# Optimization experiments

Hardware: AMD Instinct MI355X
Metric: run time of the kernel (lower is better)

## Reference

```python
import jax, jax.numpy as jnp
import numpy as np

MARGIN = 0.3
NORM_EPS = 1e-12  # torch F.normalize default eps


def setup_inputs() -> dict:
    key = jax.random.key(0)
    k1, k2 = jax.random.split(key)
    embeddings = jax.random.normal(k1, (8192, 128), dtype=jnp.float32)
    labels = jax.random.randint(k2, (8192,), 0, 128, dtype=jnp.int64)
    return {"embeddings": embeddings, "labels": labels}


def _triplet_loss(embeddings, labels):
    # L2-normalize rows (torch F.normalize: x / max(||x||, eps))
    norm = jnp.linalg.norm(embeddings, axis=1, keepdims=True)
    e = embeddings / jnp.maximum(norm, NORM_EPS)

    # pairwise squared Euclidean via gram matrix
    dot = e @ e.T                     # [B, B]
    sq = jnp.diagonal(dot)            # [B]
    d2 = jnp.clip(sq[None, :] - 2.0 * dot + sq[:, None], 0.0)
    zmask = (d2 == 0.0).astype(d2.dtype)
    dist = jnp.sqrt(d2 + zmask * 1e-16) * (1.0 - zmask)  # [B, B]

    # hard mining, fully vectorized over rows
    same = labels[:, None] == labels[None, :]
    eye = jnp.eye(labels.shape[0], dtype=bool)
    pos_mask = same & ~eye
    neg_mask = ~same

    dist_ap = jnp.max(jnp.where(pos_mask, dist, -jnp.inf), axis=1)  # hardest positive
    dist_an = jnp.min(jnp.where(neg_mask, dist, jnp.inf), axis=1)   # hardest negative

    valid = pos_mask.any(axis=1) & neg_mask.any(axis=1)
    # MarginRankingLoss(margin)(dist_an, dist_ap, y=1) = mean relu(dist_ap - dist_an + margin)
    per_row = jnp.maximum(dist_ap - dist_an + MARGIN, 0.0)
    n_valid = jnp.maximum(jnp.sum(valid), 1).astype(dist.dtype)
    loss = jnp.sum(jnp.where(valid, per_row, 0.0)) / n_valid
    return jnp.where(valid.any(), loss, jnp.zeros((), dist.dtype))


def reference(embeddings, labels):
    return _triplet_loss(embeddings, labels)
```

## Files before the change

kernel.cpp:

```cpp
#include <hip/hip_runtime.h>
#include <cmath>

#define BN 8192
#define DIM 128
#define MARGIN_F 0.3f
#define NSPLIT 8
#define CPS 1024
#define NT 8
#define IMAX 0x7FFFFFFF
#define IMIN 0x80000000

typedef __attribute__((ext_vector_type(4))) int i32x4;

__device__ __forceinline__ int imin3(int a, int b, int c) { return min(a, min(b, c)); }
__device__ __forceinline__ int imax3(int a, int b, int c) { return max(a, max(b, c)); }

__global__ __launch_bounds__(256) void norm_cvt_k(
    const float* __restrict__ emb, float* __restrict__ sqv, unsigned short* __restrict__ EnQ16,
    int* __restrict__ ap_f, int* __restrict__ an_f)
{
  int gt = blockIdx.x * blockDim.x + threadIdx.x;
  if (gt < BN) { ap_f[gt] = IMAX; an_f[gt] = IMIN; }

  int w = gt >> 6;
  int lane = threadIdx.x & 63;
  if (w >= BN) return;
  float2 v = *reinterpret_cast<const float2*>(&emb[w * DIM + lane * 2]);
  float s = v.x * v.x + v.y * v.y;
  #pragma unroll
  for (int off = 32; off > 0; off >>= 1) s += __shfl_xor(s, off);
  float iv = 1.0f / fmaxf(sqrtf(s), 1e-12f);
  if (lane == 0) sqv[w] = s * iv * iv;
  int q0 = (int)rintf(127.0f * v.x * iv);
  int q1 = (int)rintf(127.0f * v.y * iv);
  unsigned short us = (unsigned short)((q0 & 255) | ((q1 & 255) << 8));
  int g = lane >> 3;
  EnQ16[(g * BN + w) * 8 + (lane & 7)] = us;
}

__global__ __launch_bounds__(256, 2) void gram_mine_mfma_k(
    const char* __restrict__ EnQ, const int* __restrict__ lab,
    int* __restrict__ ap_f, int* __restrict__ an_f)
{
  __shared__ __align__(16) char Bs[2][16384];

  const int tid = threadIdx.x;
  const int w = tid >> 6, l = tid & 63;
  const int wr = w >> 1, wc = w & 1;
  const int lrow = l & 15, lkg = l >> 4;

  const int rowBase = blockIdx.x * 128 + wr * 64;
  const int panel   = blockIdx.y * CPS;

  i32x4 a[4][2];
  #pragma unroll
  for (int mi = 0; mi < 4; ++mi)
    #pragma unroll
    for (int kk = 0; kk < 2; ++kk)
      a[mi][kk] = *reinterpret_cast<const i32x4*>(
          EnQ + (((size_t)((kk << 2) + lkg) * BN + rowBase + mi * 16 + lrow) << 4));

  unsigned rlbp[4];
  #pragma unroll
  for (int mi = 0; mi < 4; ++mi) {
    int rb = rowBase + mi * 16 + lkg * 4;
    rlbp[mi] = (unsigned)(lab[rb] & 255) | ((unsigned)(lab[rb + 1] & 255) << 8) |
               ((unsigned)(lab[rb + 2] & 255) << 16) | ((unsigned)(lab[rb + 3] & 255) << 24);
  }

  int ap[4][4], an[4][4];
  #pragma unroll
  for (int mi = 0; mi < 4; ++mi)
    #pragma unroll
    for (int r = 0; r < 4; ++r) { ap[mi][r] = IMAX; an[mi][r] = IMIN; }

  const i32x4 zf = {0, 0, 0, 0};

  auto stage = [&](int buf, int colTile) {
    #pragma unroll
    for (int i = 0; i < 4; ++i) {
      int s0 = (w << 8) + (i << 6);
      int s  = s0 + l;
      const char* gp = EnQ + (((size_t)(s >> 7) * BN + colTile + (s & 127)) << 4);
      __builtin_amdgcn_global_load_lds(
          (const __attribute__((address_space(1))) void*)gp,
          (__attribute__((address_space(3))) void*)(&Bs[buf][s0 * 16]),
          16, 0, 0);
    }
  };

  stage(0, panel);
  __syncthreads();

  int cur = 0;
  #pragma unroll 1
  for (int ct = 0; ct < NT; ++ct) {
    const int colTile = panel + ct * 128;
    const int colBase = colTile + wc * 64;

    if (ct + 1 < NT) stage(cur ^ 1, colTile + 128);

    int clb[4];
    #pragma unroll
    for (int ni = 0; ni < 4; ++ni) clb[ni] = lab[colBase + ni * 16 + lrow];

    const bool diag = (rowBase == colBase);

    #pragma unroll
    for (int half = 0; half < 2; ++half) {
      const int n0 = half * 2, n1 = half * 2 + 1;

      i32x4 acc[4][2];
      {
        i32x4 b[2];
        #pragma unroll
        for (int n = 0; n < 2; ++n)
          b[n] = *reinterpret_cast<const i32x4*>(
              &Bs[cur][((0 + lkg) * 128 + wc * 64 + (n0 + n) * 16 + lrow) * 16]);
        #pragma unroll
        for (int mi = 0; mi < 4; ++mi)
          #pragma unroll
          for (int n = 0; n < 2; ++n)
            acc[mi][n] = __builtin_amdgcn_mfma_i32_16x16x64_i8(
                a[mi][0], b[n], zf, 0, 0, 0);
      }
      {
        i32x4 b[2];
        #pragma unroll
        for (int n = 0; n < 2; ++n)
          b[n] = *reinterpret_cast<const i32x4*>(
              &Bs[cur][((4 + lkg) * 128 + wc * 64 + (n0 + n) * 16 + lrow) * 16]);
        #pragma unroll
        for (int mi = 0; mi < 4; ++mi)
          #pragma unroll
          for (int n = 0; n < 2; ++n)
            acc[mi][n] = __builtin_amdgcn_mfma_i32_16x16x64_i8(
                a[mi][1], b[n], acc[mi][n], 0, 0, 0);
      }

      if (diag) {
        #pragma unroll
        for (int mi = 0; mi < 4; ++mi)
          #pragma unroll
          for (int r = 0; r < 4; ++r) {
            int rl = (int)((rlbp[mi] >> (r * 8)) & 255u);
            int rloc = mi * 16 + lkg * 4 + r;
            int d0 = acc[mi][0][r], d1 = acc[mi][1][r];
            bool s0 = (rl == clb[n0]), s1 = (rl == clb[n1]);
            bool e0 = (rloc == n0 * 16 + lrow), e1 = (rloc == n1 * 16 + lrow);
            int p0 = (s0 && !e0) ? d0 : IMAX;
            int p1 = (s1 && !e1) ? d1 : IMAX;
            int q0 = s0 ? IMIN : d0;
            int q1 = s1 ? IMIN : d1;
            ap[mi][r] = imin3(ap[mi][r], p0, p1);
            an[mi][r] = imax3(an[mi][r], q0, q1);
          }
      } else {
        #pragma unroll
        for (int mi = 0; mi < 4; ++mi)
          #pragma unroll
          for (int r = 0; r < 4; ++r) {
            int rl = (int)((rlbp[mi] >> (r * 8)) & 255u);
            int d0 = acc[mi][0][r], d1 = acc[mi][1][r];
            bool s0 = (rl == clb[n0]), s1 = (rl == clb[n1]);
            int p0 = s0 ? d0 : IMAX;
            int p1 = s1 ? d1 : IMAX;
            int q0 = s0 ? IMIN : d0;
            int q1 = s1 ? IMIN : d1;
            ap[mi][r] = imin3(ap[mi][r], p0, p1);
            an[mi][r] = imax3(an[mi][r], q0, q1);
          }
      }
    }

    __syncthreads();
    cur ^= 1;
  }

  #pragma unroll
  for (int mi = 0; mi < 4; ++mi)
    #pragma unroll
    for (int r = 0; r < 4; ++r) {
      int p = ap[mi][r], n = an[mi][r];
      #pragma unroll
      for (int off = 1; off < 16; off <<= 1) {
        p = min(p, __shfl_xor(p, off));
        n = max(n, __shfl_xor(n, off));
      }
      if (lrow == 0) {
        int rg = rowBase + mi * 16 + lkg * 4 + r;
        atomicMin(&ap_f[rg], p);
        atomicMax(&an_f[rg], n);
      }
    }
}

__global__ __launch_bounds__(1024) void finalize_k(
    const int* __restrict__ ap_f, const int* __restrict__ an_f,
    const float* __restrict__ sqv, float* __restrict__ out)
{
  int t = threadIdx.x;
  float sum = 0.f, cnt = 0.f;
  #pragma unroll
  for (int i = 0; i < BN / 1024; ++i) {
    int r = i * 1024 + t;
    int apt = ap_f[r], ant = an_f[r];
    if (apt != IMAX && ant != IMIN) {
      const float sc = 2.0f / (127.0f * 127.0f);
      float rs1 = sqv[r] + 1.0f;
      float dap = sqrtf(fmaxf(fmaf(-sc, (float)apt, rs1), 0.f));
      float dan = sqrtf(fmaxf(fmaf(-sc, (float)ant, rs1), 0.f));
      sum += fmaxf(dap - dan + MARGIN_F, 0.f);
      cnt += 1.f;
    }
  }
  #pragma unroll
  for (int off = 32; off > 0; off >>= 1) {
    sum += __shfl_xor(sum, off);
    cnt += __shfl_xor(cnt, off);
  }
  __shared__ float ssum[16], scnt[16];
  int wv = t >> 6;
  if ((t & 63) == 0) { ssum[wv] = sum; scnt[wv] = cnt; }
  __syncthreads();
  if (t == 0) {
    float s = 0.f, c = 0.f;
    #pragma unroll
    for (int i = 0; i < 16; ++i) { s += ssum[i]; c += scnt[i]; }
    out[0] = (c > 0.f) ? (s / c) : 0.f;
  }
}

extern "C" void kernel_launch(void* const* d_in, const int* in_sizes, int n_in,
                              void* d_out, int out_size, void* d_ws, size_t ws_size,
                              hipStream_t stream)
{
  const float* emb = (const float*)d_in[0];
  const int*   lab = (const int*)d_in[1];
  float* out = (float*)d_out;
  float* ws  = (float*)d_ws;

  float* sqv  = ws;
  int*   ap_f = (int*)(sqv + BN);
  int*   an_f = ap_f + BN;
  char*  EnQ  = (char*)(an_f + BN);

  norm_cvt_k<<<dim3(BN / 4), 256, 0, stream>>>(emb, sqv, (unsigned short*)EnQ, ap_f, an_f);
  gram_mine_mfma_k<<<dim3(BN / 128, NSPLIT), 256, 0, stream>>>(EnQ, lab, ap_f, an_f);
  finalize_k<<<dim3(1), 1024, 0, stream>>>(ap_f, an_f, sqv, out);
}
```

Before: 35.82 us.

## Counting-sort rows by label so tiles without shared labels skip positive mining

Adds a histogram kernel and scatters normalized, quantized rows into label-sorted order. In the gram kernel, each 64x64 wave tile compares its row and column label ranges, and tiles with no overlap update only the hardest-negative max, skipping label loads and comparisons. This is meant to cut the per-element mining ALU work that follows the MFMAs. In exchange it adds a serial single-block prefix kernel, atomics in the normalize kernel, and nondeterministic row order within each bin; the final mean does not depend on row order.

New measurement: 53.16 us. +48.4%, slower.

```diff
diff --git a/kernel.cpp b/kernel.cpp
--- a/kernel.cpp
+++ b/kernel.cpp
@@ -7,6 +7,7 @@
 #define NSPLIT 8
 #define CPS 1024
 #define NT 8
+#define NLAB 128
 #define IMAX 0x7FFFFFFF
 #define IMIN 0x80000000
 
@@ -15,8 +16,35 @@
 __device__ __forceinline__ int imin3(int a, int b, int c) { return min(a, min(b, c)); }
 __device__ __forceinline__ int imax3(int a, int b, int c) { return max(a, max(b, c)); }
 
+__global__ __launch_bounds__(1024) void sort_prep_k(
+    const int* __restrict__ lab, int* __restrict__ binStart, int* __restrict__ binCur)
+{
+  __shared__ int h[16][NLAB];
+  int t = threadIdx.x, wv = t >> 6;
+  for (int i = t; i < 16 * NLAB; i += 1024) (&h[0][0])[i] = 0;
+  __syncthreads();
+  for (int i = t; i < BN; i += 1024) atomicAdd(&h[wv][lab[i] & (NLAB - 1)], 1);
+  __syncthreads();
+  if (t < NLAB) {
+    int s = 0;
+    #pragma unroll
+    for (int w2 = 0; w2 < 16; ++w2) s += h[w2][t];
+    h[0][t] = s;
+  }
+  __syncthreads();
+  if (t == 0) {
+    int acc = 0;
+    for (int b = 0; b < NLAB; ++b) {
+      int c = h[0][b];
+      binStart[b] = acc; binCur[b] = acc; acc += c;
+    }
+  }
+}
+
 __global__ __launch_bounds__(256) void norm_cvt_k(
-    const float* __restrict__ emb, float* __restrict__ sqv, unsigned short* __restrict__ EnQ16,
+    const float* __restrict__ emb, const int* __restrict__ lab,
+    float* __restrict__ sqvS, unsigned short* __restrict__ EnQ16,
+    int* __restrict__ labS, int* __restrict__ binCur,
     int* __restrict__ ap_f, int* __restrict__ an_f)
 {
   int gt = blockIdx.x * blockDim.x + threadIdx.x;
@@ -25,21 +53,27 @@
   int w = gt >> 6;
   int lane = threadIdx.x & 63;
   if (w >= BN) return;
+
+  int lb = 0, dst = 0;
+  if (lane == 0) { lb = lab[w]; dst = atomicAdd(&binCur[lb], 1); }
+  dst = __shfl(dst, 0);
+  lb  = __shfl(lb, 0);
+
   float2 v = *reinterpret_cast<const float2*>(&emb[w * DIM + lane * 2]);
   float s = v.x * v.x + v.y * v.y;
   #pragma unroll
   for (int off = 32; off > 0; off >>= 1) s += __shfl_xor(s, off);
   float iv = 1.0f / fmaxf(sqrtf(s), 1e-12f);
-  if (lane == 0) sqv[w] = s * iv * iv;
+  if (lane == 0) { sqvS[dst] = s * iv * iv; labS[dst] = lb; }
   int q0 = (int)rintf(127.0f * v.x * iv);
   int q1 = (int)rintf(127.0f * v.y * iv);
   unsigned short us = (unsigned short)((q0 & 255) | ((q1 & 255) << 8));
   int g = lane >> 3;
-  EnQ16[(g * BN + w) * 8 + (lane & 7)] = us;
+  EnQ16[(g * BN + dst) * 8 + (lane & 7)] = us;
 }
 
 __global__ __launch_bounds__(256, 2) void gram_mine_mfma_k(
-    const char* __restrict__ EnQ, const int* __restrict__ lab,
+    const char* __restrict__ EnQ, const int* __restrict__ labS,
     int* __restrict__ ap_f, int* __restrict__ an_f)
 {
   __shared__ __align__(16) char Bs[2][16384];
@@ -52,6 +86,8 @@
   const int rowBase = blockIdx.x * 128 + wr * 64;
   const int panel   = blockIdx.y * CPS;
 
+  const int rLo = labS[rowBase], rHi = labS[rowBase + 63];
+
   i32x4 a[4][2];
   #pragma unroll
   for (int mi = 0; mi < 4; ++mi)
@@ -64,8 +100,8 @@
   #pragma unroll
   for (int mi = 0; mi < 4; ++mi) {
     int rb = rowBase + mi * 16 + lkg * 4;
-    rlbp[mi] = (unsigned)(lab[rb] & 255) | ((unsigned)(lab[rb + 1] & 255) << 8) |
-               ((unsigned)(lab[rb + 2] & 255) << 16) | ((unsigned)(lab[rb + 3] & 255) << 24);
+    rlbp[mi] = (unsigned)(labS[rb] & 255) | ((unsigned)(labS[rb + 1] & 255) << 8) |
+               ((unsigned)(labS[rb + 2] & 255) << 16) | ((unsigned)(labS[rb + 3] & 255) << 24);
   }
 
   int ap[4][4], an[4][4];
@@ -100,11 +136,15 @@
 
     if (ct + 1 < NT) stage(cur ^ 1, colTile + 128);
 
+    const int cLo = labS[colBase], cHi = labS[colBase + 63];
+    const bool mixed = (cHi >= rLo) && (cLo <= rHi);
+    const bool diag  = (rowBase == colBase);
+
     int clb[4];
-    #pragma unroll
-    for (int ni = 0; ni < 4; ++ni) clb[ni] = lab[colBase + ni * 16 + lrow];
-
-    const bool diag = (rowBase == colBase);
+    if (mixed) {
+      #pragma unroll
+      for (int ni = 0; ni < 4; ++ni) clb[ni] = labS[colBase + ni * 16 + lrow];
+    }
 
     #pragma unroll
     for (int half = 0; half < 2; ++half) {
@@ -138,7 +178,13 @@
                 a[mi][1], b[n], acc[mi][n], 0, 0, 0);
       }
 
-      if (diag) {
+      if (!mixed) {
+        #pragma unroll
+        for (int mi = 0; mi < 4; ++mi)
+          #pragma unroll
+          for (int r = 0; r < 4; ++r)
+            an[mi][r] = imax3(an[mi][r], acc[mi][0][r], acc[mi][1][r]);
+      } else if (diag) {
         #pragma unroll
         for (int mi = 0; mi < 4; ++mi)
           #pragma unroll
@@ -197,7 +243,7 @@
 
 __global__ __launch_bounds__(1024) void finalize_k(
     const int* __restrict__ ap_f, const int* __restrict__ an_f,
-    const float* __restrict__ sqv, float* __restrict__ out)
+    const float* __restrict__ sqvS, float* __restrict__ out)
 {
   int t = threadIdx.x;
   float sum = 0.f, cnt = 0.f;
@@ -207,7 +253,7 @@
     int apt = ap_f[r], ant = an_f[r];
     if (apt != IMAX && ant != IMIN) {
       const float sc = 2.0f / (127.0f * 127.0f);
-      float rs1 = sqv[r] + 1.0f;
+      float rs1 = sqvS[r] + 1.0f;
       float dap = sqrtf(fmaxf(fmaf(-sc, (float)apt, rs1), 0.f));
       float dan = sqrtf(fmaxf(fmaf(-sc, (float)ant, rs1), 0.f));
       sum += fmaxf(dap - dan + MARGIN_F, 0.f);
@@ -240,12 +286,17 @@
   float* out = (float*)d_out;
   float* ws  = (float*)d_ws;
 
-  float* sqv  = ws;
-  int*   ap_f = (int*)(sqv + BN);
-  int*   an_f = ap_f + BN;
-  char*  EnQ  = (char*)(an_f + BN);
-
-  norm_cvt_k<<<dim3(BN / 4), 256, 0, stream>>>(emb, sqv, (unsigned short*)EnQ, ap_f, an_f);
-  gram_mine_mfma_k<<<dim3(BN / 128, NSPLIT), 256, 0, stream>>>(EnQ, lab, ap_f, an_f);
-  finalize_k<<<dim3(1), 1024, 0, stream>>>(ap_f, an_f, sqv, out);
-}
+  float* sqvS     = ws;
+  int*   ap_f     = (int*)(sqvS + BN);
+  int*   an_f     = ap_f + BN;
+  int*   labS     = an_f + BN;
+  int*   binStart = labS + BN;
+  int*   binCur   = binStart + NLAB;
+  char*  EnQ      = (char*)(binCur + NLAB + 16);
+
+  sort_prep_k<<<dim3(1), 1024, 0, stream>>>(lab, binStart, binCur);
+  norm_cvt_k<<<dim3(BN / 4), 256, 0, stream>>>(emb, lab, sqvS, (unsigned short*)EnQ,
+                                               labS, binCur, ap_f, an_f);
+  gram_mine_mfma_k<<<dim3(BN / 128, NSPLIT), 256, 0, stream>>>(EnQ, labS, ap_f, an_f);
+  finalize_k<<<dim3(1), 1024, 0, stream>>>(ap_f, an_f, sqvS, out);
+}
```

## Exploit Gram symmetry with upper-triangular tiles and column-side mining

Applied to the files above, without the earlier changes.

Replaces the row-block by column-panel grid with one block per upper-triangular 128x128 tile pair, using the symmetry of the Gram matrix to mine both rows and columns from each tile. This roughly halves the MFMA and mining work, and each block now loads its B operand straight from global memory instead of double-buffering it through LDS. Column labels are prepacked in the normalize kernel, and atomics for empty positive sets are skipped. The cost is many more small blocks with no intra-block loop, plus extra column reductions and atomics per off-diagonal tile.

Result: slower. 56.80 us (+58.6%).

```diff
diff --git a/kernel.cpp b/kernel.cpp
--- a/kernel.cpp
+++ b/kernel.cpp
@@ -4,9 +4,8 @@
 #define BN 8192
 #define DIM 128
 #define MARGIN_F 0.3f
-#define NSPLIT 8
-#define CPS 1024
-#define NT 8
+#define NRB 64
+#define NTILE (NRB * (NRB + 1) / 2)
 #define IMAX 0x7FFFFFFF
 #define IMIN 0x80000000
 
@@ -16,11 +15,17 @@
 __device__ __forceinline__ int imax3(int a, int b, int c) { return max(a, max(b, c)); }
 
 __global__ __launch_bounds__(256) void norm_cvt_k(
-    const float* __restrict__ emb, float* __restrict__ sqv, unsigned short* __restrict__ EnQ16,
-    int* __restrict__ ap_f, int* __restrict__ an_f)
+    const float* __restrict__ emb, const int* __restrict__ lab,
+    float* __restrict__ sqv, unsigned short* __restrict__ EnQ16,
+    unsigned* __restrict__ LP, int* __restrict__ ap_f, int* __restrict__ an_f)
 {
   int gt = blockIdx.x * blockDim.x + threadIdx.x;
   if (gt < BN) { ap_f[gt] = IMAX; an_f[gt] = IMIN; }
+  if (gt < 2048) {
+    int base = (gt >> 4) * 64 + (gt & 15);
+    LP[gt] = (unsigned)(lab[base] & 255) | ((unsigned)(lab[base + 16] & 255) << 8) |
+             ((unsigned)(lab[base + 32] & 255) << 16) | ((unsigned)(lab[base + 48] & 255) << 24);
+  }
 
   int w = gt >> 6;
   int lane = threadIdx.x & 63;
@@ -38,19 +43,26 @@
   EnQ16[(g * BN + w) * 8 + (lane & 7)] = us;
 }
 
-__global__ __launch_bounds__(256, 2) void gram_mine_mfma_k(
+__global__ __launch_bounds__(256, 2) void tri_gram_mine_k(
     const char* __restrict__ EnQ, const int* __restrict__ lab,
+    const unsigned* __restrict__ LP,
     int* __restrict__ ap_f, int* __restrict__ an_f)
 {
-  __shared__ __align__(16) char Bs[2][16384];
-
   const int tid = threadIdx.x;
   const int w = tid >> 6, l = tid & 63;
   const int wr = w >> 1, wc = w & 1;
   const int lrow = l & 15, lkg = l >> 4;
 
-  const int rowBase = blockIdx.x * 128 + wr * 64;
-  const int panel   = blockIdx.y * CPS;
+  const int idx = blockIdx.x;
+  int R = (int)((129.0f - sqrtf(16641.0f - 8.0f * (float)idx)) * 0.5f);
+  while (((R + 1) * (129 - (R + 1))) / 2 <= idx) ++R;
+  while ((R * (129 - R)) / 2 > idx) --R;
+  const int C = R + (idx - (R * (129 - R)) / 2);
+
+  const int rowBase = R * 128 + wr * 64;
+  const int colBase = C * 128 + wc * 64;
+  const bool diagW  = (rowBase == colBase);
+  const bool doCol  = (R != C);
 
   i32x4 a[4][2];
   #pragma unroll
@@ -60,121 +72,117 @@
       a[mi][kk] = *reinterpret_cast<const i32x4*>(
           EnQ + (((size_t)((kk << 2) + lkg) * BN + rowBase + mi * 16 + lrow) << 4));
 
-  unsigned rlbp[4];
+  int rlv[4][4];
   #pragma unroll
   for (int mi = 0; mi < 4; ++mi) {
     int rb = rowBase + mi * 16 + lkg * 4;
-    rlbp[mi] = (unsigned)(lab[rb] & 255) | ((unsigned)(lab[rb + 1] & 255) << 8) |
-               ((unsigned)(lab[rb + 2] & 255) << 16) | ((unsigned)(lab[rb + 3] & 255) << 24);
-  }
+    #pragma unroll
+    for (int r = 0; r < 4; ++r) rlv[mi][r] = lab[rb + r] & 255;
+  }
+
+  const unsigned LPv = LP[(colBase >> 6) * 16 + lrow];
+  const int l0 = (int)(LPv & 255u),         l1 = (int)((LPv >> 8) & 255u);
+  const int l2 = (int)((LPv >> 16) & 255u), l3 = (int)(LPv >> 24);
 
   int ap[4][4], an[4][4];
   #pragma unroll
   for (int mi = 0; mi < 4; ++mi)
     #pragma unroll
     for (int r = 0; r < 4; ++r) { ap[mi][r] = IMAX; an[mi][r] = IMIN; }
+  int cmin[4], cmax[4];
+  #pragma unroll
+  for (int n = 0; n < 4; ++n) { cmin[n] = IMAX; cmax[n] = IMIN; }
 
   const i32x4 zf = {0, 0, 0, 0};
 
-  auto stage = [&](int buf, int colTile) {
-    #pragma unroll
-    for (int i = 0; i < 4; ++i) {
-      int s0 = (w << 8) + (i << 6);
-      int s  = s0 + l;
-      const char* gp = EnQ + (((size_t)(s >> 7) * BN + colTile + (s & 127)) << 4);
-      __builtin_amdgcn_global_load_lds(
-          (const __attribute__((address_space(1))) void*)gp,
-          (__attribute__((address_space(3))) void*)(&Bs[buf][s0 * 16]),
-          16, 0, 0);
-    }
+  const char* bp0 = EnQ + (((size_t)lkg * BN + colBase + lrow) << 4);
+  const char* bp1 = bp0 + ((size_t)BN << 6);
+
+  i32x4 b0[2][2], b1[2][2];
+  #pragma unroll
+  for (int n = 0; n < 2; ++n) {
+    b0[0][n] = *reinterpret_cast<const i32x4*>(bp0 + n * 256);
+    b0[1][n] = *reinterpret_cast<const i32x4*>(bp1 + n * 256);
+    b1[0][n] = *reinterpret_cast<const i32x4*>(bp0 + (2 + n) * 256);
+    b1[1][n] = *reinterpret_cast<const i32x4*>(bp1 + (2 + n) * 256);
+  }
+
+  i32x4 accA[4][2], accB[4][2];
+  #pragma unroll
+  for (int mi = 0; mi < 4; ++mi)
+    #pragma unroll
+    for (int n = 0; n < 2; ++n)
+      accA[mi][n] = __builtin_amdgcn_mfma_i32_16x16x64_i8(a[mi][0], b0[0][n], zf, 0, 0, 0);
+  #pragma unroll
+  for (int mi = 0; mi < 4; ++mi)
+    #pragma unroll
+    for (int n = 0; n < 2; ++n)
+      accA[mi][n] = __builtin_amdgcn_mfma_i32_16x16x64_i8(a[mi][1], b0[1][n], accA[mi][n], 0, 0, 0);
+  #pragma unroll
+  for (int mi = 0; mi < 4; ++mi)
+    #pragma unroll
+    for (int n = 0; n < 2; ++n)
+      accB[mi][n] = __builtin_amdgcn_mfma_i32_16x16x64_i8(a[mi][0], b1[0][n], zf, 0, 0, 0);
+  #pragma unroll
+  for (int mi = 0; mi < 4; ++mi)
+    #pragma unroll
+    for (int n = 0; n < 2; ++n)
+      accB[mi][n] = __builtin_amdgcn_mfma_i32_16x16x64_i8(a[mi][1], b1[1][n], accB[mi][n], 0, 0, 0);
+
+  auto mineRow = [&](const i32x4 (&A)[4][2], int la, int lb) {
+    #pragma unroll
+    for (int mi = 0; mi < 4; ++mi)
+      #pragma unroll
+      for (int r = 0; r < 4; ++r) {
+        int d0 = A[mi][0][r], d1 = A[mi][1][r];
+        bool s0 = (rlv[mi][r] == la), s1 = (rlv[mi][r] == lb);
+        int p0 = s0 ? d0 : IMAX, p1 = s1 ? d1 : IMAX;
+        int q0 = s0 ? IMIN : d0, q1 = s1 ? IMIN : d1;
+        ap[mi][r] = imin3(ap[mi][r], p0, p1);
+        an[mi][r] = imax3(an[mi][r], q0, q1);
+      }
   };
-
-  stage(0, panel);
-  __syncthreads();
-
-  int cur = 0;
-  #pragma unroll 1
-  for (int ct = 0; ct < NT; ++ct) {
-    const int colTile = panel + ct * 128;
-    const int colBase = colTile + wc * 64;
-
-    if (ct + 1 < NT) stage(cur ^ 1, colTile + 128);
-
-    int clb[4];
-    #pragma unroll
-    for (int ni = 0; ni < 4; ++ni) clb[ni] = lab[colBase + ni * 16 + lrow];
-
-    const bool diag = (rowBase == colBase);
-
-    #pragma unroll
-    for (int half = 0; half < 2; ++half) {
-      const int n0 = half * 2, n1 = half * 2 + 1;
-
-      i32x4 acc[4][2];
-      {
-        i32x4 b[2];
-        #pragma unroll
-        for (int n = 0; n < 2; ++n)
-          b[n] = *reinterpret_cast<const i32x4*>(
-              &Bs[cur][((0 + lkg) * 128 + wc * 64 + (n0 + n) * 16 + lrow) * 16]);
-        #pragma unroll
-        for (int mi = 0; mi < 4; ++mi)
-          #pragma unroll
-          for (int n = 0; n < 2; ++n)
-            acc[mi][n] = __builtin_amdgcn_mfma_i32_16x16x64_i8(
-                a[mi][0], b[n], zf, 0, 0, 0);
-      }
-      {
-        i32x4 b[2];
-        #pragma unroll
-        for (int n = 0; n < 2; ++n)
-          b[n] = *reinterpret_cast<const i32x4*>(
-              &Bs[cur][((4 + lkg) * 128 + wc * 64 + (n0 + n) * 16 + lrow) * 16]);
-        #pragma unroll
-        for (int mi = 0; mi < 4; ++mi)
-          #pragma unroll
-          for (int n = 0; n < 2; ++n)
-            acc[mi][n] = __builtin_amdgcn_mfma_i32_16x16x64_i8(
-                a[mi][1], b[n], acc[mi][n], 0, 0, 0);
-      }
-
-      if (diag) {
-        #pragma unroll
-        for (int mi = 0; mi < 4; ++mi)
-          #pragma unroll
-          for (int r = 0; r < 4; ++r) {
-            int rl = (int)((rlbp[mi] >> (r * 8)) & 255u);
-            int rloc = mi * 16 + lkg * 4 + r;
-            int d0 = acc[mi][0][r], d1 = acc[mi][1][r];
-            bool s0 = (rl == clb[n0]), s1 = (rl == clb[n1]);
-            bool e0 = (rloc == n0 * 16 + lrow), e1 = (rloc == n1 * 16 + lrow);
-            int p0 = (s0 && !e0) ? d0 : IMAX;
-            int p1 = (s1 && !e1) ? d1 : IMAX;
-            int q0 = s0 ? IMIN : d0;
-            int q1 = s1 ? IMIN : d1;
-            ap[mi][r] = imin3(ap[mi][r], p0, p1);
-            an[mi][r] = imax3(an[mi][r], q0, q1);
-          }
-      } else {
-        #pragma unroll
-        for (int mi = 0; mi < 4; ++mi)
-          #pragma unroll
-          for (int r = 0; r < 4; ++r) {
-            int rl = (int)((rlbp[mi] >> (r * 8)) & 255u);
-            int d0 = acc[mi][0][r], d1 = acc[mi][1][r];
-            bool s0 = (rl == clb[n0]), s1 = (rl == clb[n1]);
-            int p0 = s0 ? d0 : IMAX;
-            int p1 = s1 ? d1 : IMAX;
-            int q0 = s0 ? IMIN : d0;
-            int q1 = s1 ? IMIN : d1;
-            ap[mi][r] = imin3(ap[mi][r], p0, p1);
-            an[mi][r] = imax3(an[mi][r], q0, q1);
-          }
-      }
-    }
-
-    __syncthreads();
-    cur ^= 1;
+  auto mineRowCol = [&](const i32x4 (&A)[4][2], int la, int lb,
+                        int& cmA, int& cxA, int& cmB, int& cxB) {
+    #pragma unroll
+    for (int mi = 0; mi < 4; ++mi)
+      #pragma unroll
+      for (int r = 0; r < 4; ++r) {
+        int d0 = A[mi][0][r], d1 = A[mi][1][r];
+        bool s0 = (rlv[mi][r] == la), s1 = (rlv[mi][r] == lb);
+        int p0 = s0 ? d0 : IMAX, p1 = s1 ? d1 : IMAX;
+        int q0 = s0 ? IMIN : d0, q1 = s1 ? IMIN : d1;
+        ap[mi][r] = imin3(ap[mi][r], p0, p1);
+        an[mi][r] = imax3(an[mi][r], q0, q1);
+        cmA = min(cmA, p0); cxA = max(cxA, q0);
+        cmB = min(cmB, p1); cxB = max(cxB, q1);
+      }
+  };
+  auto mineDiag = [&](const i32x4 (&A)[4][2], int la, int lb, int c0, int c1) {
+    #pragma unroll
+    for (int mi = 0; mi < 4; ++mi)
+      #pragma unroll
+      for (int r = 0; r < 4; ++r) {
+        int rloc = mi * 16 + lkg * 4 + r;
+        int d0 = A[mi][0][r], d1 = A[mi][1][r];
+        bool s0 = (rlv[mi][r] == la), s1 = (rlv[mi][r] == lb);
+        bool e0 = (rloc == c0), e1 = (rloc == c1);
+        int p0 = (s0 && !e0) ? d0 : IMAX, p1 = (s1 && !e1) ? d1 : IMAX;
+        int q0 = s0 ? IMIN : d0, q1 = s1 ? IMIN : d1;
+        ap[mi][r] = imin3(ap[mi][r], p0, p1);
+        an[mi][r] = imax3(an[mi][r], q0, q1);
+      }
+  };
+
+  if (diagW) {
+    mineDiag(accA, l0, l1, lrow, 16 + lrow);
+    mineDiag(accB, l2, l3, 32 + lrow, 48 + lrow);
+  } else if (doCol) {
+    mineRowCol(accA, l0, l1, cmin[0], cmax[0], cmin[1], cmax[1]);
+    mineRowCol(accB, l2, l3, cmin[2], cmax[2], cmin[3], cmax[3]);
+  } else {
+    mineRow(accA, l0, l1);
+    mineRow(accB, l2, l3);
   }
 
   #pragma unroll
@@ -189,10 +197,24 @@
       }
       if (lrow == 0) {
         int rg = rowBase + mi * 16 + lkg * 4 + r;
-        atomicMin(&ap_f[rg], p);
+        if (p != IMAX) atomicMin(&ap_f[rg], p);
         atomicMax(&an_f[rg], n);
       }
     }
+
+  if (doCol) {
+    #pragma unroll
+    for (int n = 0; n < 4; ++n) {
+      int cm = cmin[n], cx = cmax[n];
+      cm = min(cm, __shfl_xor(cm, 16)); cm = min(cm, __shfl_xor(cm, 32));
+      cx = max(cx, __shfl_xor(cx, 16)); cx = max(cx, __shfl_xor(cx, 32));
+      if (lkg == 0) {
+        int cg = colBase + n * 16 + lrow;
+        if (cm != IMAX) atomicMin(&ap_f[cg], cm);
+        atomicMax(&an_f[cg], cx);
+      }
+    }
+  }
 }
 
 __global__ __launch_bounds__(1024) void finalize_k(
@@ -240,12 +262,14 @@
   float* out = (float*)d_out;
   float* ws  = (float*)d_ws;
 
-  float* sqv  = ws;
-  int*   ap_f = (int*)(sqv + BN);
-  int*   an_f = ap_f + BN;
-  char*  EnQ  = (char*)(an_f + BN);
-
-  norm_cvt_k<<<dim3(BN / 4), 256, 0, stream>>>(emb, sqv, (unsigned short*)EnQ, ap_f, an_f);
-  gram_mine_mfma_k<<<dim3(BN / 128, NSPLIT), 256, 0, stream>>>(EnQ, lab, ap_f, an_f);
+  float*    sqv  = ws;
+  int*      ap_f = (int*)(sqv + BN);
+  int*      an_f = ap_f + BN;
+  unsigned* LP   = (unsigned*)(an_f + BN);
+  char*     EnQ  = (char*)(LP + 2048);
+
+  norm_cvt_k<<<dim3(BN / 4), 256, 0, stream>>>(emb, lab, sqv, (unsigned short*)EnQ,
+                                               LP, ap_f, an_f);
+  tri_gram_mine_k<<<dim3(NTILE), 256, 0, stream>>>(EnQ, lab, LP, ap_f, an_f);
   finalize_k<<<dim3(1), 1024, 0, stream>>>(ap_f, an_f, sqv, out);
 }
```
